# Optimization experiments

Hardware: AMD Instinct MI355X
Metric: run time of the kernel (lower is better)

The kernel has to match this reference:

```python
import jax, jax.numpy as jnp
import numpy as np

NUM_THRESHOLDS = 200
N = 4_000_000
KEPS = 1e-07
EPS = 1e-06


def _make_thresholds(num_thresholds=NUM_THRESHOLDS):
    inner = [(i + 1) * 1.0 / (num_thresholds - 1) for i in range(num_thresholds - 2)]
    return jnp.asarray([0.0 - KEPS] + inner + [1.0 + KEPS], dtype=jnp.float32)


def setup_inputs() -> dict:
    key = jax.random.key(0)
    k1, k2 = jax.random.split(key)
    predictions = jax.random.uniform(k1, (N,), dtype=jnp.float32)  # in [0,1]
    labels = jax.random.randint(k2, (N,), 0, 2, dtype=jnp.int32)
    thresholds = _make_thresholds()
    return {"predictions": predictions, "labels": labels, "thresholds": thresholds}


def reference(predictions, labels, thresholds):
    # Confusion matrix at all thresholds: [T, N] broadcast compare, reduce over N.
    lab_pos = labels.astype(bool)  # [N]
    pred_pos = predictions[None, :] > thresholds[:, None]  # [T, N] bool
    lab_pos_b = jnp.broadcast_to(lab_pos[None, :], pred_pos.shape)
    tp = jnp.sum(jnp.logical_and(lab_pos_b, pred_pos), axis=1).astype(jnp.float32)
    fn = jnp.sum(jnp.logical_and(lab_pos_b, ~pred_pos), axis=1).astype(jnp.float32)
    fp = jnp.sum(jnp.logical_and(~lab_pos_b, pred_pos), axis=1).astype(jnp.float32)
    tn = jnp.sum(jnp.logical_and(~lab_pos_b, ~pred_pos), axis=1).astype(jnp.float32)
    # Trapezoidal AUC over (FPR, TPR)
    rec = (tp + EPS) / (tp + fn + EPS)          # y (TPR)
    fp_rate = fp / (fp + tn + EPS)              # x (FPR)
    x, y = fp_rate, rec
    auc = jnp.sum((x[:-1] - x[1:]) * (y[:-1] + y[1:]) * 0.5)
    return auc
```

## Files before the change

### kernel.cpp

```cpp
#include <hip/hip_runtime.h>

#define NTH    200
#define NBINS  201
#define NWAVES 4
#define NBLK   512

__global__ void __launch_bounds__(256)
auroc_hist_kernel(const float* __restrict__ preds,
                  const int*   __restrict__ labels,
                  const float* __restrict__ thresholds,
                  unsigned int* __restrict__ g_pos,
                  unsigned int* __restrict__ g_neg,
                  int n) {
    __shared__ float        s_th[NTH];
    __shared__ unsigned int s_hist[NWAVES][NBINS];

    const int t    = threadIdx.x;
    const int wave = t >> 6;

    for (int i = t; i < NWAVES * NBINS; i += 256)
        ((unsigned int*)s_hist)[i] = 0u;
    for (int i = t; i < NTH; i += 256)
        s_th[i] = thresholds[i];
    __syncthreads();

    unsigned int* my = s_hist[wave];

    const int gid    = blockIdx.x * 256 + t;
    const int stride = gridDim.x * 256;
    const int n4     = n >> 2;
    const float4* p4 = (const float4*)preds;
    const int4*   l4 = (const int4*)labels;

    for (int i = gid; i < n4; i += stride) {
        float4 p = p4[i];
        int4   l = l4[i];
        float  pv[4] = {p.x, p.y, p.z, p.w};
        int    lv[4] = {l.x, l.y, l.z, l.w};
#pragma unroll
        for (int j = 0; j < 4; ++j) {
            float pp = pv[j];
            int k0 = (int)(pp * 199.0f);
            k0 = k0 > 198 ? 198 : k0;
            float ta = s_th[k0];
            float tb = s_th[k0 + 1];
            int g = k0 + ((ta < pp) ? ((tb < pp) ? 2 : 1) : 0);
            unsigned int add = 1u | ((unsigned int)(lv[j] != 0) << 16);
            atomicAdd(&my[g], add);
        }
    }
    for (int i = (n4 << 2) + gid; i < n; i += stride) {
        float pp = preds[i];
        int k0 = (int)(pp * 199.0f);
        k0 = k0 > 198 ? 198 : k0;
        float ta = s_th[k0];
        float tb = s_th[k0 + 1];
        int g = k0 + ((ta < pp) ? ((tb < pp) ? 2 : 1) : 0);
        unsigned int add = 1u | ((unsigned int)(labels[i] != 0) << 16);
        atomicAdd(&my[g], add);
    }
    __syncthreads();

    for (int i = t; i < NBINS; i += 256) {
        unsigned int v = s_hist[0][i] + s_hist[1][i] + s_hist[2][i] + s_hist[3][i];
        unsigned int pos = v >> 16;
        unsigned int tot = v & 0xFFFFu;
        unsigned int neg = tot - pos;
        if (pos) atomicAdd(&g_pos[i], pos);
        if (neg) atomicAdd(&g_neg[i], neg);
    }
}

__global__ void __launch_bounds__(256)
auroc_finish_kernel(const unsigned int* __restrict__ g_pos,
                    const unsigned int* __restrict__ g_neg,
                    float* __restrict__ out) {
    __shared__ unsigned int s_p[NBINS];
    __shared__ unsigned int s_n[NBINS];
    __shared__ unsigned int s_sufp[NBINS + 1];
    __shared__ unsigned int s_sufn[NBINS + 1];
    __shared__ float s_x[NTH];
    __shared__ float s_y[NTH];

    const int t = threadIdx.x;
    if (t < NBINS) { s_p[t] = g_pos[t]; s_n[t] = g_neg[t]; }
    if (t == 0)    { s_sufp[NBINS] = 0u; s_sufn[NBINS] = 0u; }
    __syncthreads();

    if (t < NBINS) {
        unsigned int sp = 0u, sn = 0u;
        for (int k = t; k < NBINS; ++k) { sp += s_p[k]; sn += s_n[k]; }
        s_sufp[t] = sp;
        s_sufn[t] = sn;
    }
    __syncthreads();

    const float P   = (float)s_sufp[0];
    const float Nn  = (float)s_sufn[0];
    const float EPS = 1e-6f;

    if (t < NTH) {
        float tp = (float)s_sufp[t + 1];
        float fp = (float)s_sufn[t + 1];
        float fn = P - tp;
        float tn = Nn - fp;
        s_y[t] = (tp + EPS) / (tp + fn + EPS);
        s_x[t] = fp / (fp + tn + EPS);
    }
    __syncthreads();

    if (t == 0) {
        double auc = 0.0;
        for (int i = 0; i < NTH - 1; ++i)
            auc += (double)((s_x[i] - s_x[i + 1]) * (s_y[i] + s_y[i + 1]) * 0.5f);
        out[0] = (float)auc;
    }
}

extern "C" void kernel_launch(void* const* d_in, const int* in_sizes, int n_in,
                              void* d_out, int out_size, void* d_ws, size_t ws_size,
                              hipStream_t stream) {
    const float* preds      = (const float*)d_in[0];
    const int*   labels     = (const int*)d_in[1];
    const float* thresholds = (const float*)d_in[2];
    float*       out        = (float*)d_out;
    unsigned int* g_pos     = (unsigned int*)d_ws;
    unsigned int* g_neg     = g_pos + NBINS;

    const int n = in_sizes[0];

    hipMemsetAsync(g_pos, 0, 2 * NBINS * sizeof(unsigned int), stream);
    auroc_hist_kernel<<<NBLK, 256, 0, stream>>>(preds, labels, thresholds,
                                                g_pos, g_neg, n);
    auroc_finish_kernel<<<1, 256, 0, stream>>>(g_pos, g_neg, out);
}
```

Baseline: 101.9 us.

## Fuse memset, histogram and finish into one kernel with last-block ticket

Result: slower. 205.7 us (+101.9%).

```diff
diff --git a/kernel.cpp b/kernel.cpp
--- a/kernel.cpp
+++ b/kernel.cpp
@@ -3,20 +3,40 @@
 #define NTH    200
 #define NBINS  201
 #define NWAVES 4
-#define NBLK   512
+#define NBLK   1024
+#define MAGIC  0x9E3779B1u
 
 __global__ void __launch_bounds__(256)
-auroc_hist_kernel(const float* __restrict__ preds,
-                  const int*   __restrict__ labels,
-                  const float* __restrict__ thresholds,
-                  unsigned int* __restrict__ g_pos,
-                  unsigned int* __restrict__ g_neg,
-                  int n) {
+auroc_fused_kernel(const float* __restrict__ preds,
+                   const int*   __restrict__ labels,
+                   const float* __restrict__ thresholds,
+                   unsigned int* __restrict__ ws,
+                   float* __restrict__ out,
+                   int n) {
+    unsigned int* g_pos    = ws;
+    unsigned int* g_neg    = ws + NBINS;
+    unsigned int* g_flag   = ws + 2 * NBINS;
+    unsigned int* g_ticket = ws + 2 * NBINS + 1;
+
     __shared__ float        s_th[NTH];
     __shared__ unsigned int s_hist[NWAVES][NBINS];
+    __shared__ unsigned int s_rank;
+    __shared__ unsigned int s_p[NBINS], s_n[NBINS];
+    __shared__ unsigned int s_sufp[NBINS + 1], s_sufn[NBINS + 1];
+    __shared__ float s_x[NTH], s_y[NTH];
 
     const int t    = threadIdx.x;
     const int wave = t >> 6;
+
+    if (blockIdx.x == 0) {
+        for (int i = t; i < 2 * NBINS; i += 256) ws[i] = 0u;
+        if (t == 0) *g_ticket = 0u;
+        __syncthreads();
+        if (t == 0) {
+            __threadfence();
+            atomicExch(g_flag, MAGIC);
+        }
+    }
 
     for (int i = t; i < NWAVES * NBINS; i += 256)
         ((unsigned int*)s_hist)[i] = 0u;
@@ -61,6 +81,12 @@
     }
     __syncthreads();
 
+    if (t == 0) {
+        while (atomicAdd(g_flag, 0u) != MAGIC) {}
+    }
+    __syncthreads();
+    __threadfence();
+
     for (int i = t; i < NBINS; i += 256) {
         unsigned int v = s_hist[0][i] + s_hist[1][i] + s_hist[2][i] + s_hist[3][i];
         unsigned int pos = v >> 16;
@@ -69,22 +95,19 @@
         if (pos) atomicAdd(&g_pos[i], pos);
         if (neg) atomicAdd(&g_neg[i], neg);
     }
-}
+    __threadfence();
+    __syncthreads();
 
-__global__ void __launch_bounds__(256)
-auroc_finish_kernel(const unsigned int* __restrict__ g_pos,
-                    const unsigned int* __restrict__ g_neg,
-                    float* __restrict__ out) {
-    __shared__ unsigned int s_p[NBINS];
-    __shared__ unsigned int s_n[NBINS];
-    __shared__ unsigned int s_sufp[NBINS + 1];
-    __shared__ unsigned int s_sufn[NBINS + 1];
-    __shared__ float s_x[NTH];
-    __shared__ float s_y[NTH];
+    if (t == 0) s_rank = atomicAdd(g_ticket, 1u);
+    __syncthreads();
+    if (s_rank != (unsigned int)(gridDim.x - 1)) return;
 
-    const int t = threadIdx.x;
-    if (t < NBINS) { s_p[t] = g_pos[t]; s_n[t] = g_neg[t]; }
-    if (t == 0)    { s_sufp[NBINS] = 0u; s_sufn[NBINS] = 0u; }
+    __threadfence();
+    if (t < NBINS) {
+        s_p[t] = atomicAdd(&g_pos[t], 0u);
+        s_n[t] = atomicAdd(&g_neg[t], 0u);
+    }
+    if (t == 0) { s_sufp[NBINS] = 0u; s_sufn[NBINS] = 0u; }
     __syncthreads();
 
     if (t < NBINS) {
@@ -124,13 +147,10 @@
     const int*   labels     = (const int*)d_in[1];
     const float* thresholds = (const float*)d_in[2];
     float*       out        = (float*)d_out;
-    unsigned int* g_pos     = (unsigned int*)d_ws;
-    unsigned int* g_neg     = g_pos + NBINS;
+    unsigned int* ws        = (unsigned int*)d_ws;
 
     const int n = in_sizes[0];
 
-    hipMemsetAsync(g_pos, 0, 2 * NBINS * sizeof(unsigned int), stream);
-    auroc_hist_kernel<<<NBLK, 256, 0, stream>>>(preds, labels, thresholds,
-                                                g_pos, g_neg, n);
-    auroc_finish_kernel<<<1, 256, 0, stream>>>(g_pos, g_neg, out);
+    auroc_fused_kernel<<<NBLK, 256, 0, stream>>>(preds, labels, thresholds,
+                                                 ws, out, n);
 }
```

## Replace global atomics with per-block partial histograms and drop memset

Applied to the files above, without the earlier changes.

New measurement: 101.0 us. No clear change (-0.9%).

```diff
diff --git a/kernel.cpp b/kernel.cpp
--- a/kernel.cpp
+++ b/kernel.cpp
@@ -2,32 +2,33 @@
 
 #define NTH    200
 #define NBINS  201
-#define NWAVES 4
-#define NBLK   512
+#define NROWS  (2 * NBINS)
+#define NBLKH  256
+#define HTPB   1024
+#define HWAVES 16
 
-__global__ void __launch_bounds__(256)
+__global__ void __launch_bounds__(HTPB)
 auroc_hist_kernel(const float* __restrict__ preds,
                   const int*   __restrict__ labels,
                   const float* __restrict__ thresholds,
-                  unsigned int* __restrict__ g_pos,
-                  unsigned int* __restrict__ g_neg,
+                  unsigned int* __restrict__ part,
                   int n) {
     __shared__ float        s_th[NTH];
-    __shared__ unsigned int s_hist[NWAVES][NBINS];
+    __shared__ unsigned int s_hist[HWAVES][NBINS];
 
     const int t    = threadIdx.x;
     const int wave = t >> 6;
 
-    for (int i = t; i < NWAVES * NBINS; i += 256)
+    for (int i = t; i < HWAVES * NBINS; i += HTPB)
         ((unsigned int*)s_hist)[i] = 0u;
-    for (int i = t; i < NTH; i += 256)
+    for (int i = t; i < NTH; i += HTPB)
         s_th[i] = thresholds[i];
     __syncthreads();
 
     unsigned int* my = s_hist[wave];
 
-    const int gid    = blockIdx.x * 256 + t;
-    const int stride = gridDim.x * 256;
+    const int gid    = blockIdx.x * HTPB + t;
+    const int stride = gridDim.x * HTPB;
     const int n4     = n >> 2;
     const float4* p4 = (const float4*)preds;
     const int4*   l4 = (const int4*)labels;
@@ -61,35 +62,46 @@
     }
     __syncthreads();
 
-    for (int i = t; i < NBINS; i += 256) {
-        unsigned int v = s_hist[0][i] + s_hist[1][i] + s_hist[2][i] + s_hist[3][i];
+    const int b = blockIdx.x;
+    for (int i = t; i < NBINS; i += HTPB) {
+        unsigned int v = 0u;
+#pragma unroll
+        for (int w = 0; w < HWAVES; ++w) v += s_hist[w][i];
         unsigned int pos = v >> 16;
-        unsigned int tot = v & 0xFFFFu;
-        unsigned int neg = tot - pos;
-        if (pos) atomicAdd(&g_pos[i], pos);
-        if (neg) atomicAdd(&g_neg[i], neg);
+        unsigned int neg = (v & 0xFFFFu) - pos;
+        part[i * NBLKH + b]           = pos;
+        part[(NBINS + i) * NBLKH + b] = neg;
     }
 }
 
-__global__ void __launch_bounds__(256)
-auroc_finish_kernel(const unsigned int* __restrict__ g_pos,
-                    const unsigned int* __restrict__ g_neg,
+__global__ void __launch_bounds__(512)
+auroc_finish_kernel(const unsigned int* __restrict__ part,
                     float* __restrict__ out) {
-    __shared__ unsigned int s_p[NBINS];
-    __shared__ unsigned int s_n[NBINS];
-    __shared__ unsigned int s_sufp[NBINS + 1];
-    __shared__ unsigned int s_sufn[NBINS + 1];
-    __shared__ float s_x[NTH];
-    __shared__ float s_y[NTH];
+    __shared__ unsigned int s_row[NROWS];
+    __shared__ unsigned int s_sufp[NBINS + 1], s_sufn[NBINS + 1];
+    __shared__ float s_x[NTH], s_y[NTH];
 
     const int t = threadIdx.x;
-    if (t < NBINS) { s_p[t] = g_pos[t]; s_n[t] = g_neg[t]; }
-    if (t == 0)    { s_sufp[NBINS] = 0u; s_sufn[NBINS] = 0u; }
+
+    if (t < NROWS) {
+        const uint4* row = (const uint4*)(part + t * NBLKH);
+        unsigned int acc = 0u;
+#pragma unroll 8
+        for (int j = 0; j < NBLKH / 4; ++j) {
+            uint4 v = row[j];
+            acc += v.x + v.y + v.z + v.w;
+        }
+        s_row[t] = acc;
+    }
+    if (t == 0) { s_sufp[NBINS] = 0u; s_sufn[NBINS] = 0u; }
     __syncthreads();
 
     if (t < NBINS) {
         unsigned int sp = 0u, sn = 0u;
-        for (int k = t; k < NBINS; ++k) { sp += s_p[k]; sn += s_n[k]; }
+        for (int k = t; k < NBINS; ++k) {
+            sp += s_row[k];
+            sn += s_row[NBINS + k];
+        }
         s_sufp[t] = sp;
         s_sufn[t] = sn;
     }
@@ -124,13 +136,11 @@
     const int*   labels     = (const int*)d_in[1];
     const float* thresholds = (const float*)d_in[2];
     float*       out        = (float*)d_out;
-    unsigned int* g_pos     = (unsigned int*)d_ws;
-    unsigned int* g_neg     = g_pos + NBINS;
+    unsigned int* part      = (unsigned int*)d_ws;
 
     const int n = in_sizes[0];
 
-    hipMemsetAsync(g_pos, 0, 2 * NBINS * sizeof(unsigned int), stream);
-    auroc_hist_kernel<<<NBLK, 256, 0, stream>>>(preds, labels, thresholds,
-                                                g_pos, g_neg, n);
-    auroc_finish_kernel<<<1, 256, 0, stream>>>(g_pos, g_neg, out);
+    auroc_hist_kernel<<<NBLKH, HTPB, 0, stream>>>(preds, labels, thresholds,
+                                                  part, n);
+    auroc_finish_kernel<<<1, 512, 0, stream>>>(part, out);
 }
```
